# Kernel optimization log

Measured on AMD Instinct MI355X. Metric: run time of the kernel, lower is better.

The kernel has to match this reference:

```python
import jax, jax.numpy as jnp
import numpy as np

D = 128       # embedding_dim
BC = 64       # block_count
BS = 512      # block_size
K = 6         # main conv kernel size
OV = 2 * BC   # overlap_size
SCALE = 1.0 / np.sqrt(D).astype(np.float32)


def setup_inputs() -> dict:
    key = jax.random.key(0)
    ks = jax.random.split(key, 6)
    B = 8
    x = jax.random.normal(ks[0], (B, BC * BS, D), dtype=jnp.float32)
    w_lw = jax.random.normal(ks[1], (D, 1), dtype=jnp.float32) * 0.05
    b_lw = jnp.zeros((1,), dtype=jnp.float32)
    conv_w = jax.random.normal(ks[2], (D, D, K), dtype=jnp.float32) * 0.05  # (out, in, k)
    conv_b = jnp.zeros((D,), dtype=jnp.float32)
    fusion_w = jax.random.normal(ks[3], (3 * D, D), dtype=jnp.float32) * 0.05
    fusion_b = jnp.zeros((D,), dtype=jnp.float32)
    return {"x": x, "w_lw": w_lw, "b_lw": b_lw, "conv_w": conv_w,
            "conv_b": conv_b, "fusion_w": fusion_w, "fusion_b": fusion_b}


def _prefix_softmax_weighted_sum(x, logits):
    # x: (B, L, D), logits: (B, L) -- faithful replica of the torch scan
    pmax = jax.lax.cummax(logits, axis=1)
    ex = jnp.exp(logits - pmax)                    # (B, L)
    psum = jnp.cumsum(ex, axis=1)                  # (B, L)
    wpre = jnp.cumsum(ex[..., None] * x, axis=1)   # (B, L, D)
    return wpre / psum[..., None]


def _attn(q, k, v):
    # q: (N, 1, D); k, v: (N, S, D)
    s = jnp.einsum('nqd,nkd->nqk', q, k) * SCALE
    return jnp.einsum('nqk,nkd->nqd', jax.nn.softmax(s, axis=-1), v)


def reference(x, w_lw, b_lw, conv_w, conv_b, fusion_w, fusion_b):
    B, L, _ = x.shape  # L == BC * BS, so F.pad in the original is a no-op
    logits = jax.nn.silu(x @ w_lw + b_lw)[..., 0]          # (B, L)
    prefix_x = _prefix_softmax_weighted_sum(x, logits) + x  # (B, L, D)

    # per-block conv1d (kernel 6, padding='same' in torch => pad (2,3))
    blocks = prefix_x.reshape(B * BC, BS, D).transpose(0, 2, 1)  # (N, D, BS)
    conv = jax.lax.conv_general_dilated(
        blocks, conv_w, window_strides=(1,), padding=[(2, 3)],
        dimension_numbers=('NCH', 'OIH', 'NCH')) + conv_b[None, :, None]
    blocks_c = conv.transpose(0, 2, 1)                           # (N, BS, D)
    block_repr = jnp.max(blocks_c, axis=1)[:, None, :]           # (N, 1, D)

    # overlap windows: replicate-pad end by OV//2, slice, gather OV-wide windows
    xov = jnp.pad(prefix_x, ((0, 0), (0, OV // 2), (0, 0)), mode='edge')
    xov = xov[:, BS - OV // 2:, :]                               # (B, (BC-1)*BS + OV, D)
    idx = (jnp.arange(BC) * BS)[:, None] + jnp.arange(OV)[None, :]  # (BC, OV)
    xbo = xov[:, idx, :].reshape(B * BC, OV, D)

    a_s = _attn(block_repr, blocks_c, blocks_c)  # block->self
    a_o = _attn(block_repr, xbo, xbo)            # block->overlap
    fused = jnp.concatenate([a_s, a_o, block_repr], axis=-1)    # (N, 1, 3D)
    out = (fused @ fusion_w + fusion_b).reshape(B, BC, D)
    return (out, out)
```

## Files before the change

### kernel.cpp

```cpp
#include <hip/hip_runtime.h>
#include <hip/hip_bf16.h>

#define NB 8
#define LSEQ 32768
#define DCH 128
#define NCHUNK 1024
#define NSUB 4096
#define NBLK 512
#define PH 520
#define SCALE_F 0.08838834764831845f

typedef __bf16 bf16x8 __attribute__((ext_vector_type(8)));
typedef float f32x4 __attribute__((ext_vector_type(4)));

__device__ __forceinline__ float bf2f(unsigned short u) {
    return __uint_as_float(((unsigned)u) << 16);
}
__device__ __forceinline__ unsigned short f2bf(float f) {
    unsigned u = __float_as_uint(f);
    u += 0x7fffu + ((u >> 16) & 1u);
    return (unsigned short)(u >> 16);
}

__device__ __forceinline__ void async_copy16(const void* gsrc, void* ldst) {
    __builtin_amdgcn_global_load_lds(
        (const __attribute__((address_space(1))) unsigned int*)gsrc,
        (__attribute__((address_space(3))) unsigned int*)ldst, 16, 0, 0);
}


__global__ __launch_bounds__(256) void k_logits2(const float* __restrict__ x,
                                                 const float* __restrict__ w_lw,
                                                 const float* __restrict__ b_lw,
                                                 float* __restrict__ logits,
                                                 float* __restrict__ subM) {
    int chunk = blockIdx.x, t = threadIdx.x;
    int g = t & 15, rs = t >> 4;
    __shared__ float sp[256 * 17];
    __shared__ float red[256];
    float wv[8];
    #pragma unroll
    for (int e = 0; e < 8; ++e) wv[e] = w_lw[g * 8 + e];
    float bb = b_lw[0];
    size_t base = (size_t)chunk * 256 * DCH;
    for (int i = 0; i < 16; ++i) {
        int row = rs * 16 + i;
        float4 a  = *(const float4*)(x + base + (size_t)row * DCH + g * 8);
        float4 b4 = *(const float4*)(x + base + (size_t)row * DCH + g * 8 + 4);
        sp[row * 17 + g] = a.x * wv[0] + a.y * wv[1] + a.z * wv[2] + a.w * wv[3] +
                           b4.x * wv[4] + b4.y * wv[5] + b4.z * wv[6] + b4.w * wv[7];
    }
    __syncthreads();
    float s = bb;
    #pragma unroll
    for (int j = 0; j < 16; ++j) s += sp[t * 17 + j];
    float l = s / (1.f + expf(-s));
    logits[(size_t)chunk * 256 + t] = l;
    red[t] = l;
    __syncthreads();
    for (int off = 32; off >= 1; off >>= 1) {
        if ((t & 63) < off) red[t] = fmaxf(red[t], red[t + off]);
        __syncthreads();
    }
    if ((t & 63) == 0) subM[chunk * 4 + (t >> 6)] = red[t];
}

__global__ __launch_bounds__(64) void k_seed_max2(const float* __restrict__ subM,
                                                  float* __restrict__ seedM) {
    int b = blockIdx.x, lane = threadIdx.x;
    const float* src = subM + b * 512;
    float* dst = seedM + b * 512;
    float v[8];
    float m = -INFINITY;
    #pragma unroll
    for (int j = 0; j < 8; ++j) { v[j] = src[lane * 8 + j]; m = fmaxf(m, v[j]); }
    float incl = m;
    #pragma unroll
    for (int off = 1; off < 64; off <<= 1) {
        float o = __shfl_up(incl, off, 64);
        if (lane >= off) incl = fmaxf(incl, o);
    }
    float ex = __shfl_up(incl, 1, 64);
    if (lane == 0) ex = -INFINITY;
    float run = ex;
    #pragma unroll
    for (int j = 0; j < 8; ++j) { dst[lane * 8 + j] = run; run = fmaxf(run, v[j]); }
}

__global__ __launch_bounds__(256) void k_sums(const float* __restrict__ x,
                                              const float* __restrict__ logits,
                                              const float* __restrict__ seedM,
                                              float* __restrict__ exg,
                                              float* __restrict__ S_w,
                                              float* __restrict__ S_wx) {
    int chunk = blockIdx.x, t = threadIdx.x;
    int g = t & 15, rs = t >> 4;
    int w = t >> 6, lane = t & 63;
    __shared__ float wbuf[256];
    __shared__ float red[256];
    __shared__ float rp[16 * 130];
    float l = logits[(size_t)chunk * 256 + t];
    float M = seedM[chunk * 4 + w];
    float incl = l;
    #pragma unroll
    for (int off = 1; off < 64; off <<= 1) {
        float o = __shfl_up(incl, off, 64);
        if (lane >= off) incl = fmaxf(incl, o);
    }
    float w_t = expf(l - fmaxf(M, incl));
    wbuf[t] = w_t;
    exg[(size_t)chunk * 256 + t] = w_t;
    red[t] = w_t;
    __syncthreads();
    for (int off = 32; off >= 1; off >>= 1) {
        if ((t & 63) < off) red[t] += red[t + off];
        __syncthreads();
    }
    if ((t & 63) == 0) S_w[chunk * 4 + (t >> 6)] = red[t];
    float acc[8];
    #pragma unroll
    for (int e = 0; e < 8; ++e) acc[e] = 0.f;
    size_t base = (size_t)chunk * 256 * DCH;
    for (int i = 0; i < 16; ++i) {
        int row = rs * 16 + i;
        float ww = wbuf[row];
        float4 a  = *(const float4*)(x + base + (size_t)row * DCH + g * 8);
        float4 b4 = *(const float4*)(x + base + (size_t)row * DCH + g * 8 + 4);
        acc[0] += ww * a.x;  acc[1] += ww * a.y;  acc[2] += ww * a.z;  acc[3] += ww * a.w;
        acc[4] += ww * b4.x; acc[5] += ww * b4.y; acc[6] += ww * b4.z; acc[7] += ww * b4.w;
    }
    #pragma unroll
    for (int e = 0; e < 8; ++e) rp[rs * 130 + g * 8 + e] = acc[e];
    __syncthreads();
    #pragma unroll
    for (int k = 0; k < 2; ++k) {
        int idx = k * 256 + t;
        int sub = idx >> 7, c = idx & 127;
        float sm = rp[(sub * 4 + 0) * 130 + c] + rp[(sub * 4 + 1) * 130 + c] +
                   rp[(sub * 4 + 2) * 130 + c] + rp[(sub * 4 + 3) * 130 + c];
        S_wx[((size_t)chunk * 4 + sub) * DCH + c] = sm;
    }
}

__global__ __launch_bounds__(256) void k_seed_both(const float* __restrict__ S_w,
                                                   float* __restrict__ sS_w,
                                                   const float* __restrict__ S_wx,
                                                   float* __restrict__ sS_wx) {
    int blk = blockIdx.x, t = threadIdx.x;
    if (blk < 8) {
        if (t < 64) {
            const float* src = S_w + blk * 512;
            float* dst = sS_w + blk * 512;
            float v[8];
            float tot = 0.f;
            #pragma unroll
            for (int j = 0; j < 8; ++j) { v[j] = src[t * 8 + j]; tot += v[j]; }
            float incl = tot;
            #pragma unroll
            for (int off = 1; off < 64; off <<= 1) {
                float o = __shfl_up(incl, off, 64);
                if (t >= off) incl += o;
            }
            float ex = __shfl_up(incl, 1, 64);
            if (t == 0) ex = 0.f;
            float run = ex;
            #pragma unroll
            for (int j = 0; j < 8; ++j) { dst[t * 8 + j] = run; run += v[j]; }
        }
        return;
    }
    int b = (blk - 8) >> 3, cgx = (blk - 8) & 7;
    int cl = t & 15, seg = t >> 4;
    int c = cgx * 16 + cl;
    __shared__ float tots[16][17];
    const float* src = S_wx + (size_t)b * 512 * DCH + c;
    float* dst = sS_wx + (size_t)b * 512 * DCH + c;
    int s0 = seg * 32;
    float tot = 0.f;
    for (int j = 0; j < 32; ++j) tot += src[(size_t)(s0 + j) * DCH];
    tots[seg][cl] = tot;
    __syncthreads();
    if (t < 16) {
        float run = 0.f;
        for (int s = 0; s < 16; ++s) { float tmp = tots[s][t]; tots[s][t] = run; run += tmp; }
    }
    __syncthreads();
    float run = tots[seg][cl];
    for (int j = 0; j < 32; ++j) {
        float val = src[(size_t)(s0 + j) * DCH];
        dst[(size_t)(s0 + j) * DCH] = run;
        run += val;
    }
}

__global__ __launch_bounds__(256) void k_init(const float* __restrict__ conv_w,
                                              unsigned short* __restrict__ W3,
                                              unsigned short* __restrict__ P) {
    int n = blockIdx.x, t = threadIdx.x;
    for (int i = t; i < 1024; i += 256) {
        int rr = i >> 7;
        int row = (rr < 2) ? rr : 512 + rr;
        P[(n * PH + row) * DCH + (i & 127)] = 0;
    }
    int idx = n * 256 + t;
    if (idx < 98304) {
        int e  = idx & 7;
        int o  = (idx >> 3) & 127;
        int kc = (idx >> 10) & 3;
        int kt2 = idx >> 12;
        int kt = kt2 >> 1, ks = kt2 & 1;
        int i  = (kt & 1) * 64 + (ks * 4 + kc) * 8 + e;
        int kn = kt >> 1;
        W3[idx] = f2bf(conv_w[(o * 128 + i) * 6 + kn]);
    }
}

__global__ __launch_bounds__(256) void k_apply(const float* __restrict__ x,
                                               const float* __restrict__ exg,
                                               const float* __restrict__ sS_w,
                                               const float* __restrict__ sS_wx,
                                               unsigned short* __restrict__ P) {
    int t = threadIdx.x, w = t >> 6, lane = t & 63;
    int s = blockIdx.x * 4 + w;
    int b = s >> 9, sb = s & 511;
    __shared__ float e2[256];
    e2[t] = exg[(size_t)blockIdx.x * 256 + t];
    float2 axx = *(const float2*)(sS_wx + (size_t)s * DCH + 2 * lane);
    float aex = sS_w[s];
    __syncthreads();
    const float* es = e2 + w * 64;
    int pib0 = sb * 64;
    int n = b * 64 + (pib0 >> 9);
    int row0 = (pib0 & 511) + 2;
    const float* xp = x + ((size_t)b * LSEQ + pib0) * DCH + 2 * lane;
    unsigned short* pp = P + ((size_t)n * PH + row0) * DCH + 2 * lane;
    for (int j = 0; j < 64; ++j) {
        float e = es[j];
        aex += e;
        float2 xv = *(const float2*)xp;
        axx.x += e * xv.x;
        axx.y += e * xv.y;
        float inv = __builtin_amdgcn_rcpf(aex);
        unsigned pk = ((unsigned)f2bf(axx.y * inv + xv.y) << 16) | f2bf(axx.x * inv + xv.x);
        *(unsigned*)pp = pk;
        xp += DCH;
        pp += DCH;
    }
}

__global__ __launch_bounds__(256) void k_conv(const unsigned short* __restrict__ P,
                                              const unsigned short* __restrict__ W3,
                                              const float* __restrict__ conv_b,
                                              unsigned short* __restrict__ convout,
                                              float* __restrict__ brpart) {
    int n = blockIdx.x >> 2;
    int h0 = (blockIdx.x & 3) * 128;
    __shared__ __align__(16) char panel[144 * 256];
    int t = threadIdx.x;
    int wave = t >> 6, lane = t & 63;
    f32x4 acc[4][4] = {};
    const unsigned short* Pn = P + (size_t)n * PH * DCH;
    int wm = (wave >> 1) * 64, wn = (wave & 1) * 64;
    int kchunk = lane >> 4;
    int bcol = wn + (lane & 15);

    bf16x8 breg[2][8];

    auto loadB = [&](int kt, bf16x8* dstB) {
        #pragma unroll
        for (int ks = 0; ks < 2; ++ks)
            #pragma unroll
            for (int ni = 0; ni < 4; ++ni)
                dstB[ks * 4 + ni] = *(const bf16x8*)(
                    W3 + (size_t)((kt * 2 + ks) * 4 + kchunk) * 1024 + (bcol + ni * 16) * 8);
    };

    {
        int c = lane & 15;
        #pragma unroll
        for (int j = 0; j < 9; ++j) {
            int r = j * 16 + wave * 4 + (lane >> 4);
            int gr = h0 + r;
            int grc = min(gr, PH - 1);
            int srcc = (c & 8) | ((c & 7) ^ (gr & 7));
            async_copy16(Pn + (size_t)grc * DCH + srcc * 8,
                         panel + j * 4096 + wave * 1024 + lane * 16);
        }
    }
    loadB(0, breg[0]);
    __syncthreads();

    #pragma unroll
    for (int kt = 0; kt < 12; ++kt) {
        if (kt < 11) loadB(kt + 1, breg[(kt + 1) & 1]);
        int kn = kt >> 1;
        int cb = (kt & 1) * 8;
        #pragma unroll
        for (int ks = 0; ks < 2; ++ks) {
            bf16x8 af[4];
            #pragma unroll
            for (int mi = 0; mi < 4; ++mi) {
                int row = wm + mi * 16 + (lane & 15) + kn;
                int phys = cb + ((ks * 4 + kchunk) ^ ((h0 + row) & 7));
                af[mi] = *(const bf16x8*)(panel + row * 256 + phys * 16);
            }
            __builtin_amdgcn_s_setprio(1);
            #pragma unroll
            for (int mi = 0; mi < 4; ++mi)
                #pragma unroll
                for (int ni = 0; ni < 4; ++ni)
                    acc[mi][ni] = __builtin_amdgcn_mfma_f32_16x16x32_bf16(af[mi],
                                                                          breg[kt & 1][ks * 4 + ni],
                                                                          acc[mi][ni], 0, 0, 0);
            __builtin_amdgcn_s_setprio(0);
        }
    }

    float* part = (float*)(panel + 35840);
    {
        #pragma unroll
        for (int ni = 0; ni < 4; ++ni) {
            float pm = -INFINITY;
            #pragma unroll
            for (int mi = 0; mi < 4; ++mi)
                #pragma unroll
                for (int r = 0; r < 4; ++r) pm = fmaxf(pm, acc[mi][ni][r]);
            pm = fmaxf(pm, __shfl_xor(pm, 16, 64));
            pm = fmaxf(pm, __shfl_xor(pm, 32, 64));
            if (lane < 16) part[wave * 64 + ni * 16 + lane] = pm;
        }
    }
    __syncthreads();
    if (t < 128) {
        int c = t;
        int w0 = c >> 6;
        float pm2 = fmaxf(part[w0 * 64 + (c & 63)], part[(w0 + 2) * 64 + (c & 63)]);
        brpart[((size_t)n * 4 + (blockIdx.x & 3)) * DCH + c] = pm2 + conv_b[c];
    }
    unsigned short* clds = (unsigned short*)panel;
    #pragma unroll
    for (int mi = 0; mi < 4; ++mi)
        #pragma unroll
        for (int ni = 0; ni < 4; ++ni) {
            int col = wn + ni * 16 + (lane & 15);
            float bias = conv_b[col];
            #pragma unroll
            for (int r = 0; r < 4; ++r) {
                int row = wm + mi * 16 + (lane >> 4) * 4 + r;
                clds[row * 136 + col] = f2bf(acc[mi][ni][r] + bias);
            }
        }
    __syncthreads();
    size_t base = (size_t)(n * 512 + h0) * DCH;
    #pragma unroll
    for (int it = 0; it < 8; ++it) {
        int idx = it * 256 + t;
        int row = idx >> 4, g = idx & 15;
        uint4 v = *(const uint4*)(clds + row * 136 + g * 8);
        *(uint4*)(convout + base + (size_t)row * DCH + g * 8) = v;
    }
}

__global__ __launch_bounds__(256) void k_tail(const unsigned short* __restrict__ conv,
                                              const unsigned short* __restrict__ P,
                                              const float* __restrict__ brpart,
                                              const float* __restrict__ fusion_w,
                                              const float* __restrict__ fusion_b,
                                              float* __restrict__ block_repr,
                                              float* __restrict__ out) {
    int n = blockIdx.x, t = threadIdx.x;
    int g = t & 15, rs = t >> 4;
    int b = n >> 6, c = n & 63;
    __shared__ __align__(16) float sp[512 * 17];
    __shared__ float s[512];
    __shared__ float br[128];
    __shared__ float as_l[128];
    __shared__ float ao_l[128];
    __shared__ float red[128];
    __shared__ int rb[128];
    float* rp = sp;
    const unsigned short* base = conv + (size_t)n * 512 * DCH;

    if (t < 128) {
        const float* bp = brpart + (size_t)n * 4 * DCH + t;
        float bm = fmaxf(fmaxf(bp[0], bp[DCH]), fmaxf(bp[2 * DCH], bp[3 * DCH]));
        float bmv = bf2f(f2bf(bm));
        br[t] = bmv;
        block_repr[n * DCH + t] = bmv;
    }
    __syncthreads();

    float brv[8];
    #pragma unroll
    for (int e = 0; e < 8; ++e) brv[e] = br[g * 8 + e];
    for (int i = 0; i < 32; ++i) {
        int row = i * 16 + rs;
        uint4 v = *(const uint4*)(base + row * DCH + g * 8);
        unsigned vv[4] = {v.x, v.y, v.z, v.w};
        float p = 0.f;
        #pragma unroll
        for (int e = 0; e < 4; ++e) {
            p += bf2f((unsigned short)(vv[e] & 0xffff)) * brv[2 * e];
            p += bf2f((unsigned short)(vv[e] >> 16))    * brv[2 * e + 1];
        }
        sp[row * 17 + g] = p;
    }
    __syncthreads();
    #pragma unroll
    for (int rr = 0; rr < 2; ++rr) {
        int row = t * 2 + rr;
        float p = 0.f;
        #pragma unroll
        for (int j = 0; j < 16; ++j) p += sp[row * 17 + j];
        s[row] = p * SCALE_F;
    }
    __syncthreads();

    float* redA = sp;
    float mm = fmaxf(s[t], s[t + 256]);
    __syncthreads();
    redA[t] = mm;
    __syncthreads();
    for (int off = 128; off > 0; off >>= 1) {
        if (t < off) redA[t] = fmaxf(redA[t], redA[t + off]);
        __syncthreads();
    }
    float smax = redA[0];
    __syncthreads();
    float e0 = expf(s[t] - smax), e1 = expf(s[t + 256] - smax);
    redA[t] = e0 + e1;
    __syncthreads();
    for (int off = 128; off > 0; off >>= 1) {
        if (t < off) redA[t] += redA[t + off];
        __syncthreads();
    }
    float inv = 1.f / redA[0];
    __syncthreads();
    s[t] = e0 * inv;
    s[t + 256] = e1 * inv;
    __syncthreads();

    float acc[8];
    #pragma unroll
    for (int e = 0; e < 8; ++e) acc[e] = 0.f;
    for (int i = 0; i < 32; ++i) {
        int row = i * 16 + rs;
        float w = s[row];
        uint4 v = *(const uint4*)(base + row * DCH + g * 8);
        unsigned vv[4] = {v.x, v.y, v.z, v.w};
        #pragma unroll
        for (int e = 0; e < 4; ++e) {
            acc[2 * e]     += w * bf2f((unsigned short)(vv[e] & 0xffff));
            acc[2 * e + 1] += w * bf2f((unsigned short)(vv[e] >> 16));
        }
    }
    #pragma unroll
    for (int e = 0; e < 8; ++e) rp[rs * 130 + g * 8 + e] = acc[e];
    __syncthreads();
    if (t < 128) {
        float p = 0.f;
        #pragma unroll
        for (int r2 = 0; r2 < 16; ++r2) p += rp[r2 * 130 + t];
        as_l[t] = p;
    }

    if (t < 128) {
        int pib = (c + 1) * 512 - 64 + t;
        pib = min(pib, LSEQ - 1);
        int n2 = b * 64 + (pib >> 9);
        int row = (pib & 511) + 2;
        rb[t] = (n2 * PH + row) * DCH;
    }
    __syncthreads();
    #pragma unroll
    for (int r = 0; r < 8; ++r) {
        int row = rs * 8 + r;
        uint4 v = *(const uint4*)(P + rb[row] + g * 8);
        unsigned vv[4] = {v.x, v.y, v.z, v.w};
        float p = 0.f;
        #pragma unroll
        for (int e = 0; e < 4; ++e) {
            p += bf2f((unsigned short)(vv[e] & 0xffff)) * brv[2 * e];
            p += bf2f((unsigned short)(vv[e] >> 16))    * brv[2 * e + 1];
        }
        sp[row * 17 + g] = p;
    }
    __syncthreads();
    if (t < 128) {
        float p = 0.f;
        #pragma unroll
        for (int j = 0; j < 16; ++j) p += sp[t * 17 + j];
        s[t] = p * SCALE_F;
        red[t] = s[t];
    }
    __syncthreads();
    for (int off = 64; off > 0; off >>= 1) {
        if (t < off) red[t] = fmaxf(red[t], red[t + off]);
        __syncthreads();
    }
    float smaxB = red[0];
    __syncthreads();
    if (t < 128) {
        float e = expf(s[t] - smaxB);
        s[t] = e;
        red[t] = e;
    }
    __syncthreads();
    for (int off = 64; off > 0; off >>= 1) {
        if (t < off) red[t] += red[t + off];
        __syncthreads();
    }
    float invB = 1.f / red[0];
    __syncthreads();
    if (t < 128) s[t] *= invB;
    __syncthreads();
    float accB[8];
    #pragma unroll
    for (int e = 0; e < 8; ++e) accB[e] = 0.f;
    #pragma unroll
    for (int r = 0; r < 8; ++r) {
        int row = rs * 8 + r;
        float w = s[row];
        uint4 v = *(const uint4*)(P + rb[row] + g * 8);
        unsigned vv[4] = {v.x, v.y, v.z, v.w};
        #pragma unroll
        for (int e = 0; e < 4; ++e) {
            accB[2 * e]     += w * bf2f((unsigned short)(vv[e] & 0xffff));
            accB[2 * e + 1] += w * bf2f((unsigned short)(vv[e] >> 16));
        }
    }
    #pragma unroll
    for (int e = 0; e < 8; ++e) sp[rs * 130 + g * 8 + e] = accB[e];
    __syncthreads();
    if (t < 128) {
        float p = 0.f;
        #pragma unroll
        for (int r2 = 0; r2 < 16; ++r2) p += sp[r2 * 130 + t];
        ao_l[t] = p;
    }
    __syncthreads();

    float* fu = sp + 8320;
    if (t < 128) {
        fu[t] = as_l[t];
        fu[128 + t] = ao_l[t];
        fu[256 + t] = br[t];
    }
    __syncthreads();
    {
        int col = t & 127, h = t >> 7;
        float a2 = (h == 0) ? fusion_b[col] : 0.f;
        for (int j = h * 192; j < h * 192 + 192; ++j)
            a2 += fu[j] * fusion_w[j * DCH + col];
        sp[h * 128 + col] = a2;
    }
    __syncthreads();
    if (t < 128) {
        float v = sp[t] + sp[128 + t];
        out[n * DCH + t] = v;
        out[NB * 64 * DCH + n * DCH + t] = v;
    }
}

extern "C" void kernel_launch(void* const* d_in, const int* in_sizes, int n_in,
                              void* d_out, int out_size, void* d_ws, size_t ws_size,
                              hipStream_t stream) {
    const float* x        = (const float*)d_in[0];
    const float* w_lw     = (const float*)d_in[1];
    const float* b_lw     = (const float*)d_in[2];
    const float* conv_w   = (const float*)d_in[3];
    const float* conv_b   = (const float*)d_in[4];
    const float* fusion_w = (const float*)d_in[5];
    const float* fusion_b = (const float*)d_in[6];
    float* out = (float*)d_out;

    char* ws = (char*)d_ws;
    size_t off = 0;
    auto alloc = [&](size_t bytes) { char* p = ws + off; off += (bytes + 255) & ~(size_t)255; return p; };
    float* logits     = (float*)alloc(NB * LSEQ * 4);
    float* exg        = (float*)alloc(NB * LSEQ * 4);
    float* subM       = (float*)alloc(NSUB * 4);
    float* seedM      = (float*)alloc(NSUB * 4);
    float* S_w        = (float*)alloc(NSUB * 4);
    float* sS_w       = (float*)alloc(NSUB * 4);
    float* S_wx       = (float*)alloc((size_t)NSUB * DCH * 4);
    float* sS_wx      = (float*)alloc((size_t)NSUB * DCH * 4);
    float* block_repr = (float*)alloc(NBLK * DCH * 4);
    float* brpart     = (float*)alloc((size_t)NBLK * 4 * DCH * 4);
    unsigned short* W3      = (unsigned short*)alloc(128 * 768 * 2);
    unsigned short* P       = (unsigned short*)alloc((size_t)NBLK * PH * DCH * 2);
    unsigned short* convout = (unsigned short*)alloc((size_t)NBLK * 512 * DCH * 2);

    k_init<<<NBLK, 256, 0, stream>>>(conv_w, W3, P);
    k_logits2<<<NCHUNK, 256, 0, stream>>>(x, w_lw, b_lw, logits, subM);
    k_seed_max2<<<NB, 64, 0, stream>>>(subM, seedM);
    k_sums<<<NCHUNK, 256, 0, stream>>>(x, logits, seedM, exg, S_w, S_wx);
    k_seed_both<<<72, 256, 0, stream>>>(S_w, sS_w, S_wx, sS_wx);
    k_apply<<<NSUB / 4, 256, 0, stream>>>(x, exg, sS_w, sS_wx, P);
    k_conv<<<NBLK * 4, 256, 0, stream>>>(P, W3, conv_b, convout, brpart);
    k_tail<<<NBLK, 256, 0, stream>>>(convout, P, brpart, fusion_w, fusion_b, block_repr, out);
}
```

Before: 342.8 us.

## Fuse logits, max-scan and weighted sums into one decoupled-lookback kernel

Replaces the three-kernel sequence (logits, seed max scan, weighted sums) with a single kernel. Blocks take a dynamic virtual id from an atomic counter and run a decoupled-lookback prefix-max scan over 64-row sub-chunks. Each x tile is now read from global memory once instead of twice, and two launches go away, along with the logits and subM round trips. The cost is cross-block spin-waiting on flags, plus a flag/counter reset in k_init. It also drops the unused block_repr global write.

Measured after the change: 682.9 us. +99.2%, slower.

```diff
diff --git a/kernel.cpp b/kernel.cpp
--- a/kernel.cpp
+++ b/kernel.cpp
@@ -4,7 +4,6 @@
 #define NB 8
 #define LSEQ 32768
 #define DCH 128
-#define NCHUNK 1024
 #define NSUB 4096
 #define NBLK 512
 #define PH 520
@@ -29,116 +28,124 @@
 }
 
 
-__global__ __launch_bounds__(256) void k_logits2(const float* __restrict__ x,
-                                                 const float* __restrict__ w_lw,
-                                                 const float* __restrict__ b_lw,
-                                                 float* __restrict__ logits,
-                                                 float* __restrict__ subM) {
-    int chunk = blockIdx.x, t = threadIdx.x;
-    int g = t & 15, rs = t >> 4;
-    __shared__ float sp[256 * 17];
-    __shared__ float red[256];
-    float wv[8];
-    #pragma unroll
-    for (int e = 0; e < 8; ++e) wv[e] = w_lw[g * 8 + e];
-    float bb = b_lw[0];
-    size_t base = (size_t)chunk * 256 * DCH;
-    for (int i = 0; i < 16; ++i) {
-        int row = rs * 16 + i;
-        float4 a  = *(const float4*)(x + base + (size_t)row * DCH + g * 8);
-        float4 b4 = *(const float4*)(x + base + (size_t)row * DCH + g * 8 + 4);
-        sp[row * 17 + g] = a.x * wv[0] + a.y * wv[1] + a.z * wv[2] + a.w * wv[3] +
-                           b4.x * wv[4] + b4.y * wv[5] + b4.z * wv[6] + b4.w * wv[7];
-    }
-    __syncthreads();
-    float s = bb;
-    #pragma unroll
-    for (int j = 0; j < 16; ++j) s += sp[t * 17 + j];
-    float l = s / (1.f + expf(-s));
-    logits[(size_t)chunk * 256 + t] = l;
-    red[t] = l;
-    __syncthreads();
-    for (int off = 32; off >= 1; off >>= 1) {
-        if ((t & 63) < off) red[t] = fmaxf(red[t], red[t + off]);
+__global__ __launch_bounds__(256) void k_fls(const float* __restrict__ x,
+                                             const float* __restrict__ w_lw,
+                                             const float* __restrict__ b_lw,
+                                             float* __restrict__ exg,
+                                             float* __restrict__ S_w,
+                                             float* __restrict__ S_wx,
+                                             int* __restrict__ flags,
+                                             float* __restrict__ aggM,
+                                             float* __restrict__ inclM,
+                                             int* __restrict__ vcnt) {
+    __shared__ __align__(16) float xl[64 * 132];
+    __shared__ float lw[128];
+    __shared__ float lbuf[64];
+    __shared__ float wrow[64];
+    __shared__ float halfbuf[128];
+    __shared__ int vid_s;
+    int t = threadIdx.x;
+    if (t == 0) vid_s = atomicAdd(vcnt, 1);
+    if (t < 128) lw[t] = w_lw[t];
+    __syncthreads();
+    int s = vid_s;
+    if (s >= NSUB) return;
+    int sb = s & 511;
+    const float* xs = x + (size_t)s * 64 * DCH;
+    #pragma unroll
+    for (int i = 0; i < 8; ++i) {
+        int idx = i * 256 + t;
+        int r = idx >> 5, c4 = idx & 31;
+        float4 v = *(const float4*)(xs + (size_t)r * DCH + c4 * 4);
+        *(float4*)(xl + r * 132 + c4 * 4) = v;
+    }
+    __syncthreads();
+    {
+        int r = t >> 2, q = t & 3;
+        float p = 0.f;
+        #pragma unroll
+        for (int j = 0; j < 32; ++j) p += xl[r * 132 + q + 4 * j] * lw[q + 4 * j];
+        p += __shfl_xor(p, 1, 64);
+        p += __shfl_xor(p, 2, 64);
+        if (q == 0) lbuf[r] = p;
+    }
+    __syncthreads();
+    if (t < 64) {
+        float l = lbuf[t] + b_lw[0];
+        l = l / (1.f + expf(-l));
+        float incl = l;
+        #pragma unroll
+        for (int off = 1; off < 64; off <<= 1) {
+            float o = __shfl_up(incl, off, 64);
+            if (t >= off) incl = fmaxf(incl, o);
+        }
+        float m_i = incl;
+        float agg = __shfl(incl, 63, 64);
+        float M = -INFINITY;
+        if (sb == 0) {
+            if (t == 0) {
+                __hip_atomic_store(&inclM[s], agg, __ATOMIC_RELAXED, __HIP_MEMORY_SCOPE_AGENT);
+                __hip_atomic_store(&flags[s], 2, __ATOMIC_RELEASE, __HIP_MEMORY_SCOPE_AGENT);
+            }
+        } else {
+            if (t == 0) {
+                __hip_atomic_store(&aggM[s], agg, __ATOMIC_RELAXED, __HIP_MEMORY_SCOPE_AGENT);
+                __hip_atomic_store(&flags[s], 1, __ATOMIC_RELEASE, __HIP_MEMORY_SCOPE_AGENT);
+            }
+            int bs = s - sb;
+            int p = s - 1;
+            while (true) {
+                int idx = p - t;
+                bool valid = idx >= bs;
+                int f = 2;
+                if (valid) f = __hip_atomic_load(&flags[idx], __ATOMIC_ACQUIRE, __HIP_MEMORY_SCOPE_AGENT);
+                if (__ballot(valid && f == 0)) { __builtin_amdgcn_s_sleep(4); continue; }
+                float val;
+                if (f == 2)
+                    val = valid ? __hip_atomic_load(&inclM[idx], __ATOMIC_RELAXED, __HIP_MEMORY_SCOPE_AGENT)
+                                : -INFINITY;
+                else
+                    val = __hip_atomic_load(&aggM[idx], __ATOMIC_RELAXED, __HIP_MEMORY_SCOPE_AGENT);
+                unsigned long long incls = __ballot(f == 2);
+                if (incls) {
+                    int d = __ffsll((long long)incls) - 1;
+                    float contrib = (t <= d) ? val : -INFINITY;
+                    #pragma unroll
+                    for (int off = 32; off >= 1; off >>= 1)
+                        contrib = fmaxf(contrib, __shfl_xor(contrib, off, 64));
+                    M = fmaxf(M, contrib);
+                    break;
+                } else {
+                    float contrib = val;
+                    #pragma unroll
+                    for (int off = 32; off >= 1; off >>= 1)
+                        contrib = fmaxf(contrib, __shfl_xor(contrib, off, 64));
+                    M = fmaxf(M, contrib);
+                    p -= 64;
+                }
+            }
+            if (t == 0) {
+                __hip_atomic_store(&inclM[s], fmaxf(M, agg), __ATOMIC_RELAXED, __HIP_MEMORY_SCOPE_AGENT);
+                __hip_atomic_store(&flags[s], 2, __ATOMIC_RELEASE, __HIP_MEMORY_SCOPE_AGENT);
+            }
+        }
+        float w_t = expf(l - fmaxf(M, m_i));
+        wrow[t] = w_t;
+        exg[(size_t)s * 64 + t] = w_t;
+        float red = w_t;
+        #pragma unroll
+        for (int off = 32; off >= 1; off >>= 1) red += __shfl_xor(red, off, 64);
+        if (t == 0) S_w[s] = red;
+    }
+    __syncthreads();
+    {
+        int c = t & 127, h = t >> 7;
+        float acc = 0.f;
+        for (int r = h * 32; r < h * 32 + 32; ++r)
+            acc += wrow[r] * xl[r * 132 + c];
+        if (h == 1) halfbuf[c] = acc;
         __syncthreads();
-    }
-    if ((t & 63) == 0) subM[chunk * 4 + (t >> 6)] = red[t];
-}
-
-__global__ __launch_bounds__(64) void k_seed_max2(const float* __restrict__ subM,
-                                                  float* __restrict__ seedM) {
-    int b = blockIdx.x, lane = threadIdx.x;
-    const float* src = subM + b * 512;
-    float* dst = seedM + b * 512;
-    float v[8];
-    float m = -INFINITY;
-    #pragma unroll
-    for (int j = 0; j < 8; ++j) { v[j] = src[lane * 8 + j]; m = fmaxf(m, v[j]); }
-    float incl = m;
-    #pragma unroll
-    for (int off = 1; off < 64; off <<= 1) {
-        float o = __shfl_up(incl, off, 64);
-        if (lane >= off) incl = fmaxf(incl, o);
-    }
-    float ex = __shfl_up(incl, 1, 64);
-    if (lane == 0) ex = -INFINITY;
-    float run = ex;
-    #pragma unroll
-    for (int j = 0; j < 8; ++j) { dst[lane * 8 + j] = run; run = fmaxf(run, v[j]); }
-}
-
-__global__ __launch_bounds__(256) void k_sums(const float* __restrict__ x,
-                                              const float* __restrict__ logits,
-                                              const float* __restrict__ seedM,
-                                              float* __restrict__ exg,
-                                              float* __restrict__ S_w,
-                                              float* __restrict__ S_wx) {
-    int chunk = blockIdx.x, t = threadIdx.x;
-    int g = t & 15, rs = t >> 4;
-    int w = t >> 6, lane = t & 63;
-    __shared__ float wbuf[256];
-    __shared__ float red[256];
-    __shared__ float rp[16 * 130];
-    float l = logits[(size_t)chunk * 256 + t];
-    float M = seedM[chunk * 4 + w];
-    float incl = l;
-    #pragma unroll
-    for (int off = 1; off < 64; off <<= 1) {
-        float o = __shfl_up(incl, off, 64);
-        if (lane >= off) incl = fmaxf(incl, o);
-    }
-    float w_t = expf(l - fmaxf(M, incl));
-    wbuf[t] = w_t;
-    exg[(size_t)chunk * 256 + t] = w_t;
-    red[t] = w_t;
-    __syncthreads();
-    for (int off = 32; off >= 1; off >>= 1) {
-        if ((t & 63) < off) red[t] += red[t + off];
-        __syncthreads();
-    }
-    if ((t & 63) == 0) S_w[chunk * 4 + (t >> 6)] = red[t];
-    float acc[8];
-    #pragma unroll
-    for (int e = 0; e < 8; ++e) acc[e] = 0.f;
-    size_t base = (size_t)chunk * 256 * DCH;
-    for (int i = 0; i < 16; ++i) {
-        int row = rs * 16 + i;
-        float ww = wbuf[row];
-        float4 a  = *(const float4*)(x + base + (size_t)row * DCH + g * 8);
-        float4 b4 = *(const float4*)(x + base + (size_t)row * DCH + g * 8 + 4);
-        acc[0] += ww * a.x;  acc[1] += ww * a.y;  acc[2] += ww * a.z;  acc[3] += ww * a.w;
-        acc[4] += ww * b4.x; acc[5] += ww * b4.y; acc[6] += ww * b4.z; acc[7] += ww * b4.w;
-    }
-    #pragma unroll
-    for (int e = 0; e < 8; ++e) rp[rs * 130 + g * 8 + e] = acc[e];
-    __syncthreads();
-    #pragma unroll
-    for (int k = 0; k < 2; ++k) {
-        int idx = k * 256 + t;
-        int sub = idx >> 7, c = idx & 127;
-        float sm = rp[(sub * 4 + 0) * 130 + c] + rp[(sub * 4 + 1) * 130 + c] +
-                   rp[(sub * 4 + 2) * 130 + c] + rp[(sub * 4 + 3) * 130 + c];
-        S_wx[((size_t)chunk * 4 + sub) * DCH + c] = sm;
+        if (h == 0) S_wx[(size_t)s * DCH + c] = acc + halfbuf[c];
     }
 }
 
@@ -195,13 +202,16 @@
 
 __global__ __launch_bounds__(256) void k_init(const float* __restrict__ conv_w,
                                               unsigned short* __restrict__ W3,
-                                              unsigned short* __restrict__ P) {
+                                              unsigned short* __restrict__ P,
+                                              int* __restrict__ lbk) {
     int n = blockIdx.x, t = threadIdx.x;
     for (int i = t; i < 1024; i += 256) {
         int rr = i >> 7;
         int row = (rr < 2) ? rr : 512 + rr;
         P[(n * PH + row) * DCH + (i & 127)] = 0;
     }
+    int fi = n * 256 + t;
+    if (fi <= NSUB) lbk[fi] = 0;
     int idx = n * 256 + t;
     if (idx < 98304) {
         int e  = idx & 7;
@@ -366,7 +376,6 @@
                                               const float* __restrict__ brpart,
                                               const float* __restrict__ fusion_w,
                                               const float* __restrict__ fusion_b,
-                                              float* __restrict__ block_repr,
                                               float* __restrict__ out) {
     int n = blockIdx.x, t = threadIdx.x;
     int g = t & 15, rs = t >> 4;
@@ -384,9 +393,7 @@
     if (t < 128) {
         const float* bp = brpart + (size_t)n * 4 * DCH + t;
         float bm = fmaxf(fmaxf(bp[0], bp[DCH]), fmaxf(bp[2 * DCH], bp[3 * DCH]));
-        float bmv = bf2f(f2bf(bm));
-        br[t] = bmv;
-        block_repr[n * DCH + t] = bmv;
+        br[t] = bf2f(f2bf(bm));
     }
     __syncthreads();
 
@@ -577,26 +584,26 @@
     char* ws = (char*)d_ws;
     size_t off = 0;
     auto alloc = [&](size_t bytes) { char* p = ws + off; off += (bytes + 255) & ~(size_t)255; return p; };
-    float* logits     = (float*)alloc(NB * LSEQ * 4);
     float* exg        = (float*)alloc(NB * LSEQ * 4);
-    float* subM       = (float*)alloc(NSUB * 4);
-    float* seedM      = (float*)alloc(NSUB * 4);
     float* S_w        = (float*)alloc(NSUB * 4);
     float* sS_w       = (float*)alloc(NSUB * 4);
     float* S_wx       = (float*)alloc((size_t)NSUB * DCH * 4);
     float* sS_wx      = (float*)alloc((size_t)NSUB * DCH * 4);
-    float* block_repr = (float*)alloc(NBLK * DCH * 4);
     float* brpart     = (float*)alloc((size_t)NBLK * 4 * DCH * 4);
+    float* aggM       = (float*)alloc(NSUB * 4);
+    float* inclM      = (float*)alloc(NSUB * 4);
+    int*   lbk        = (int*)alloc((NSUB + 1) * 4);
     unsigned short* W3      = (unsigned short*)alloc(128 * 768 * 2);
     unsigned short* P       = (unsigned short*)alloc((size_t)NBLK * PH * DCH * 2);
     unsigned short* convout = (unsigned short*)alloc((size_t)NBLK * 512 * DCH * 2);
 
-    k_init<<<NBLK, 256, 0, stream>>>(conv_w, W3, P);
-    k_logits2<<<NCHUNK, 256, 0, stream>>>(x, w_lw, b_lw, logits, subM);
-    k_seed_max2<<<NB, 64, 0, stream>>>(subM, seedM);
-    k_sums<<<NCHUNK, 256, 0, stream>>>(x, logits, seedM, exg, S_w, S_wx);
+    int* flags = lbk;
+    int* vcnt  = lbk + NSUB;
+
+    k_init<<<NBLK, 256, 0, stream>>>(conv_w, W3, P, lbk);
+    k_fls<<<NSUB, 256, 0, stream>>>(x, w_lw, b_lw, exg, S_w, S_wx, flags, aggM, inclM, vcnt);
     k_seed_both<<<72, 256, 0, stream>>>(S_w, sS_w, S_wx, sS_wx);
     k_apply<<<NSUB / 4, 256, 0, stream>>>(x, exg, sS_w, sS_wx, P);
     k_conv<<<NBLK * 4, 256, 0, stream>>>(P, W3, conv_b, convout, brpart);
-    k_tail<<<NBLK, 256, 0, stream>>>(convout, P, brpart, fusion_w, fusion_b, block_repr, out);
-}
+    k_tail<<<NBLK, 256, 0, stream>>>(convout, P, brpart, fusion_w, fusion_b, out);
+}
```
